# Optimization experiments

Measured on AMD Instinct MI355X. Metric: run time of the kernel, lower is better.

The kernel has to match this reference:

```python
import jax, jax.numpy as jnp
import numpy as np

B, I, H, MS, M = 8192, 1024, 1024, 64, 16
TAU = 1.0


def setup_inputs() -> dict:
    key = jax.random.key(0)
    ks = jax.random.split(key, 24)
    s = 0.02
    eps = 1e-6
    return {
        "x": jax.random.normal(ks[0], (B, I), jnp.float32),
        "h": jax.random.normal(ks[1], (B, H), jnp.float32),
        "c": jax.random.normal(ks[2], (B, H), jnp.float32),
        "memory": jax.random.normal(ks[3], (B, M, MS), jnp.float32),
        "u_gs": jax.random.uniform(ks[4], (B, M), jnp.float32, eps, 1.0 - eps),
        "u_a": jax.random.uniform(ks[5], (B, 1), jnp.float32, eps, 1.0 - eps),
        "u_b": jax.random.uniform(ks[6], (B, 1), jnp.float32, eps, 1.0 - eps),
        # pre-concatenated gate weights, matching torch.cat((W_x2*, W_h2*, W_c2*), 0)
        "W_i": jax.random.normal(ks[7], (I + 2 * H, H), jnp.float32) * s,
        "b_i": jnp.zeros((H,), jnp.float32),
        "W_f": jax.random.normal(ks[8], (I + 2 * H, H), jnp.float32) * s,
        "b_f": jnp.ones((H,), jnp.float32),
        "W_o": jax.random.normal(ks[9], (I + 2 * H, H), jnp.float32) * s,
        "b_o": jnp.zeros((H,), jnp.float32),
        "W_cand": jax.random.normal(ks[10], (I + H, H), jnp.float32) * s,
        "b_cand": jnp.zeros((H,), jnp.float32),
        "W_m": jax.random.normal(ks[11], (H, MS), jnp.float32) * s,
        "b_m": jnp.zeros((MS,), jnp.float32),
        "w_a_h": jax.random.normal(ks[12], (H, 1), jnp.float32) * s,
        "w_a_x": jax.random.normal(ks[13], (I, 1), jnp.float32) * s,
        "w_a_r": jax.random.normal(ks[14], (MS, 1), jnp.float32) * s,
        "w_b_h": jax.random.normal(ks[15], (H, 1), jnp.float32) * s,
        "w_b_x": jax.random.normal(ks[16], (I, 1), jnp.float32) * s,
        "w_b_r": jax.random.normal(ks[17], (MS, 1), jnp.float32) * s,
    }


def reference(x, h, c, memory, u_gs, u_a, u_b,
              W_i, b_i, W_f, b_f, W_o, b_o, W_cand, b_cand,
              W_m, b_m, w_a_h, w_a_x, w_a_r, w_b_h, w_b_x, w_b_r):
    # LSTM-style gates with peephole c in the concatenated input
    xhc = jnp.concatenate([x, h, c], axis=1)            # [B, I+2H]
    i = jax.nn.sigmoid(xhc @ W_i + b_i)
    f = jax.nn.sigmoid(xhc @ W_f + b_f)
    cp = jnp.tanh(jnp.concatenate([x, h], axis=1) @ W_cand + b_cand)
    c_new = f * c + i * cp
    o = jax.nn.sigmoid(jnp.concatenate([x, h, c_new], axis=1) @ W_o + b_o)
    h_new = o * jnp.tanh(c_new)

    # memory-slot attention with Gumbel-softmax sampling
    micro = h_new @ W_m + b_m                           # [B, MS]
    logits = jnp.einsum('bmk,bk->bm', memory, micro)    # [B, M]
    g = -jnp.log(-jnp.log(u_gs))                        # Gumbel(0,1)
    attn = jax.nn.softmax((logits + g) / TAU, axis=-1)  # sampled_locations
    sampled = jnp.einsum('bmk,bm->bk', memory, attn) + 1.0  # [B, MS]

    # gumbel-sigmoid (binary concrete) for alpha / beta
    la = jnp.log(u_a) - jnp.log1p(-u_a)
    lb = jnp.log(u_b) - jnp.log1p(-u_b)
    alpha = jax.nn.sigmoid((h_new @ w_a_h + x @ w_a_x + sampled @ w_a_r + la) / TAU)
    beta = jax.nn.sigmoid((h_new @ w_b_h + x @ w_b_x + sampled @ w_b_r + lb) / TAU)

    # [B, 2H+2]
    return jnp.concatenate([h_new, c_new, alpha, beta], axis=1)
```

## Files before the change

kernel.cpp:

```cpp
#include <hip/hip_runtime.h>

typedef __bf16 bfrag __attribute__((ext_vector_type(8)));
typedef float f32x4 __attribute__((ext_vector_type(4)));

#define GLDS16(g, l) __builtin_amdgcn_global_load_lds( \
    (__attribute__((address_space(1))) void*)(g),      \
    (__attribute__((address_space(3))) void*)(l), 16, 0, 0)

__device__ __forceinline__ float bf2f(ushort u) {
    return __uint_as_float(((unsigned)u) << 16);
}
__device__ __forceinline__ ushort f2bf(float f) {
    unsigned u = __float_as_uint(f);
    u += 0x7fff + ((u >> 16) & 1);
    return (ushort)(u >> 16);
}
__device__ __forceinline__ float sigmoidf_(float v) {
    return 1.0f / (1.0f + expf(-v));
}

struct TD { const float* src; ushort* dst; int src_ld; int dst_ld; int ktiles; int off; };
struct TA { TD d[6]; };

__global__ __launch_bounds__(256) void k_prep(const float* __restrict__ x,
                                              const float* __restrict__ h,
                                              const float* __restrict__ c,
                                              ushort* __restrict__ xhcb, TA a,
                                              const float* __restrict__ bi,
                                              const float* __restrict__ bf_,
                                              const float* __restrict__ bc,
                                              const float* __restrict__ bo,
                                              float* __restrict__ Biasf) {
    __shared__ float tile[64][65];
    int bid = blockIdx.x;
    int t = threadIdx.x;
    if (bid < 12288) {
        int idx = bid * 256 + t;
        int row = idx / 384;
        int c8 = (idx - row * 384) * 8;
        const float* s = (c8 < 1024) ? &x[(size_t)row * 1024 + c8]
                       : (c8 < 2048) ? &h[(size_t)row * 1024 + (c8 - 1024)]
                                     : &c[(size_t)row * 1024 + (c8 - 2048)];
        float4 va = *(const float4*)s;
        float4 vb = *(const float4*)(s + 4);
        ushort tmp[8] = {f2bf(va.x), f2bf(va.y), f2bf(va.z), f2bf(va.w),
                         f2bf(vb.x), f2bf(vb.y), f2bf(vb.z), f2bf(vb.w)};
        *(uint4*)&xhcb[(size_t)idx * 8] = *(uint4*)tmp;
    } else if (bid < 15120) {
        int tb = bid - 12288;
        int ri = 0;
#pragma unroll
        for (int i = 1; i < 6; ++i) ri = (tb >= a.d[i].off) ? i : ri;
        const float* src = a.d[ri].src;
        ushort* dst = a.d[ri].dst;
        int src_ld = a.d[ri].src_ld, dst_ld = a.d[ri].dst_ld;
        int local = tb - a.d[ri].off;
        int bx = local % a.d[ri].ktiles;
        int by = local / a.d[ri].ktiles;
        int k0 = bx * 64, n0 = by * 64;
        int c4 = (t & 15) * 4;
        int r = t >> 4;
#pragma unroll
        for (int i = 0; i < 4; ++i) {
            int rr = r + i * 16;
            float4 v = *(const float4*)&src[(size_t)(k0 + rr) * src_ld + n0 + c4];
            tile[rr][c4 + 0] = v.x; tile[rr][c4 + 1] = v.y;
            tile[rr][c4 + 2] = v.z; tile[rr][c4 + 3] = v.w;
        }
        __syncthreads();
        int kk8 = (t & 7) * 8;
        int nn = t >> 3;
#pragma unroll
        for (int i = 0; i < 2; ++i) {
            int n = nn + i * 32;
            ushort tmp[8];
#pragma unroll
            for (int j = 0; j < 8; ++j) tmp[j] = f2bf(tile[kk8 + j][n]);
            *(uint4*)&dst[(size_t)(n0 + n) * dst_ld + k0 + kk8] = *(uint4*)tmp;
        }
    } else {
        int idx = (bid - 15120) * 256 + t;
        int g = idx >> 10, n = idx & 1023;
        const float* s = (g == 0) ? bi : (g == 1) ? bf_ : (g == 2) ? bc : bo;
        Biasf[idx] = s[n];
    }
}

template <int KTOT>
__global__ __launch_bounds__(256) void k_gemm1t(const ushort* __restrict__ xhcb,
                                                const ushort* __restrict__ WT,
                                                const float* __restrict__ bias,
                                                ushort* __restrict__ Pre, int nbase) {
    __shared__ __align__(16) ushort As[128 * 64];
    __shared__ __align__(16) ushort Bs[128 * 64];
    int t = threadIdx.x;
    int m0 = blockIdx.x * 128, n0 = nbase + blockIdx.y * 128;
    int w = t >> 6, l = t & 63;
    int wm = (w & 1) * 64, wn = (w >> 1) * 64;
    int lane16 = l & 15, quad = l >> 4;
    int rowt = t >> 3;
    int kg = (t & 7) ^ (rowt & 7);
    int r7 = lane16 & 7;
    f32x4 acc[4][4] = {};

    const ushort* Abase = xhcb + (size_t)(m0 + rowt) * 3072 + kg * 8;
    const ushort* Bbase = WT + (size_t)(n0 + rowt) * 3072 + kg * 8;

    for (int k0 = 0; k0 < KTOT; k0 += 64) {
#pragma unroll
        for (int q = 0; q < 4; ++q)
            GLDS16(Abase + (size_t)q * 32 * 3072 + k0, As + q * 2048 + t * 8);
#pragma unroll
        for (int q = 0; q < 4; ++q)
            GLDS16(Bbase + (size_t)q * 32 * 3072 + k0, Bs + q * 2048 + t * 8);
        __syncthreads();
#pragma unroll
        for (int hh = 0; hh < 2; ++hh) {
            int slot8 = ((hh * 4 + quad) ^ r7) * 8;
            bfrag af[4], bfr[4];
#pragma unroll
            for (int i = 0; i < 4; ++i) {
                af[i]  = *(const bfrag*)&As[(wm + i * 16 + lane16) * 64 + slot8];
                bfr[i] = *(const bfrag*)&Bs[(wn + i * 16 + lane16) * 64 + slot8];
            }
#pragma unroll
            for (int i = 0; i < 4; ++i)
#pragma unroll
                for (int j = 0; j < 4; ++j)
                    acc[i][j] = __builtin_amdgcn_mfma_f32_16x16x32_bf16(af[i], bfr[j], acc[i][j], 0, 0, 0);
        }
        __syncthreads();
    }
#pragma unroll
    for (int i = 0; i < 4; ++i) {
#pragma unroll
        for (int j = 0; j < 4; ++j) {
            int col = n0 + wn + j * 16 + lane16;
            float bv = bias[col];
            int rbase = m0 + wm + i * 16 + quad * 4;
#pragma unroll
            for (int r = 0; r < 4; ++r)
                Pre[(size_t)(rbase + r) * 4096 + col] = f2bf(acc[i][j][r] + bv);
        }
    }
}

__global__ __launch_bounds__(256) void k_cnew(const ushort* __restrict__ Pre,
                                              const float* __restrict__ cin,
                                              ushort* __restrict__ Cnewb,
                                              float* __restrict__ out) {
    int idx8 = blockIdx.x * 256 + threadIdx.x;
    int b = idx8 >> 7;
    int n8 = (idx8 & 127) * 8;
    uint4 vi = *(const uint4*)(Pre + (size_t)b * 4096 + n8);
    uint4 vf = *(const uint4*)(Pre + (size_t)b * 4096 + 1024 + n8);
    uint4 vc = *(const uint4*)(Pre + (size_t)b * 4096 + 2048 + n8);
    float4 c0 = *(const float4*)(cin + (size_t)b * 1024 + n8);
    float4 c1 = *(const float4*)(cin + (size_t)b * 1024 + n8 + 4);
    const ushort* pi = (const ushort*)&vi;
    const ushort* pf = (const ushort*)&vf;
    const ushort* pc = (const ushort*)&vc;
    float cv[8] = {c0.x, c0.y, c0.z, c0.w, c1.x, c1.y, c1.z, c1.w};
    float cn[8];
    ushort cb[8];
#pragma unroll
    for (int j = 0; j < 8; ++j) {
        float iv = sigmoidf_(bf2f(pi[j]));
        float fv = sigmoidf_(bf2f(pf[j]));
        float cp = tanhf(bf2f(pc[j]));
        cn[j] = fv * cv[j] + iv * cp;
        cb[j] = f2bf(cn[j]);
    }
    *(uint4*)(Cnewb + (size_t)b * 1024 + n8) = *(uint4*)cb;
    float* orow = out + (size_t)b * 2050 + 1024 + n8;
#pragma unroll
    for (int j = 0; j < 4; ++j)
        *(float2*)(orow + j * 2) = make_float2(cn[j * 2], cn[j * 2 + 1]);
}

__global__ __launch_bounds__(256) void k_gemm2(const ushort* __restrict__ Cnewb,
                                               const ushort* __restrict__ WoCT,
                                               const ushort* __restrict__ Pre,
                                               ushort* __restrict__ Hnewb,
                                               float* __restrict__ out) {
    __shared__ __align__(16) ushort As[128 * 64];
    __shared__ __align__(16) ushort Bs[128 * 64];
    int t = threadIdx.x;
    int m0 = blockIdx.x * 128, n0 = blockIdx.y * 128;
    int w = t >> 6, l = t & 63;
    int wm = (w & 1) * 64, wn = (w >> 1) * 64;
    int lane16 = l & 15, quad = l >> 4;
    int rowt = t >> 3;
    int kg = (t & 7) ^ (rowt & 7);
    int r7 = lane16 & 7;
    f32x4 acc[4][4] = {};

    const ushort* Abase = Cnewb + (size_t)(m0 + rowt) * 1024 + kg * 8;
    const ushort* Bbase = WoCT + (size_t)(n0 + rowt) * 1024 + kg * 8;

    for (int k0 = 0; k0 < 1024; k0 += 64) {
#pragma unroll
        for (int q = 0; q < 4; ++q)
            GLDS16(Abase + (size_t)q * 32 * 1024 + k0, As + q * 2048 + t * 8);
#pragma unroll
        for (int q = 0; q < 4; ++q)
            GLDS16(Bbase + (size_t)q * 32 * 1024 + k0, Bs + q * 2048 + t * 8);
        __syncthreads();
#pragma unroll
        for (int hh = 0; hh < 2; ++hh) {
            int slot8 = ((hh * 4 + quad) ^ r7) * 8;
            bfrag af[4], bfr[4];
#pragma unroll
            for (int i = 0; i < 4; ++i) {
                af[i]  = *(const bfrag*)&As[(wm + i * 16 + lane16) * 64 + slot8];
                bfr[i] = *(const bfrag*)&Bs[(wn + i * 16 + lane16) * 64 + slot8];
            }
#pragma unroll
            for (int i = 0; i < 4; ++i)
#pragma unroll
                for (int j = 0; j < 4; ++j)
                    acc[i][j] = __builtin_amdgcn_mfma_f32_16x16x32_bf16(af[i], bfr[j], acc[i][j], 0, 0, 0);
        }
        __syncthreads();
    }
#pragma unroll
    for (int i = 0; i < 4; ++i) {
#pragma unroll
        for (int j = 0; j < 4; ++j) {
            int col = n0 + wn + j * 16 + lane16;
            int rbase = m0 + wm + i * 16 + quad * 4;
#pragma unroll
            for (int r = 0; r < 4; ++r) {
                int row = rbase + r;
                float opre = acc[i][j][r] + bf2f(Pre[(size_t)row * 4096 + 3072 + col]);
                float o = sigmoidf_(opre);
                float cnv = bf2f(Cnewb[(size_t)row * 1024 + col]);
                float hv = o * tanhf(cnv);
                Hnewb[(size_t)row * 1024 + col] = f2bf(hv);
                out[(size_t)row * 2050 + col] = hv;
            }
        }
    }
}

__global__ __launch_bounds__(256) void k_attn(
    const ushort* __restrict__ Hnewb, const float* __restrict__ outr,
    const float* __restrict__ x, const float* __restrict__ memory,
    const float* __restrict__ u_gs, const float* __restrict__ u_a,
    const float* __restrict__ u_b, const ushort* __restrict__ WmT,
    const float* __restrict__ b_m,
    const float* __restrict__ w_a_h, const float* __restrict__ w_a_x,
    const float* __restrict__ w_a_r, const float* __restrict__ w_b_h,
    const float* __restrict__ w_b_x, const float* __restrict__ w_b_r,
    float* __restrict__ out) {
    __shared__ float sMicro[16 * 64];
    __shared__ float sAttn[16 * 16];
    __shared__ float sSamp[16 * 64];

    int b0 = blockIdx.x * 16;
    int t = threadIdx.x;
    int w = t >> 6, l = t & 63;
    int lane16 = l & 15, quad = l >> 4;

    {
        f32x4 acc = {0.f, 0.f, 0.f, 0.f};
        const ushort* Ab = Hnewb + (size_t)(b0 + lane16) * 1024 + quad * 8;
        const ushort* Bb = WmT + (size_t)(w * 16 + lane16) * 1024 + quad * 8;
#pragma unroll 4
        for (int k0 = 0; k0 < 1024; k0 += 32) {
            bfrag av = *(const bfrag*)(Ab + k0);
            bfrag bv = *(const bfrag*)(Bb + k0);
            acc = __builtin_amdgcn_mfma_f32_16x16x32_bf16(av, bv, acc, 0, 0, 0);
        }
        float bm = b_m[w * 16 + lane16];
#pragma unroll
        for (int r = 0; r < 4; ++r)
            sMicro[(quad * 4 + r) * 64 + w * 16 + lane16] = acc[r] + bm;
    }
    __syncthreads();

    {
        int r = t >> 4, m = t & 15;
        const float4* mem4 = (const float4*)(memory + (size_t)(b0 + r) * 1024 + m * 64);
        float lg = 0.f;
#pragma unroll
        for (int k4 = 0; k4 < 16; ++k4) {
            float4 mv = mem4[k4];
            const float* sm = &sMicro[r * 64 + k4 * 4];
            lg += mv.x * sm[0] + mv.y * sm[1] + mv.z * sm[2] + mv.w * sm[3];
        }
        float u = u_gs[(b0 + r) * 16 + m];
        float z = lg - logf(-logf(u));
        float zm = z;
        for (int off = 8; off; off >>= 1) zm = fmaxf(zm, __shfl_xor(zm, off, 16));
        float p = expf(z - zm);
        float ps = p;
        for (int off = 8; off; off >>= 1) ps += __shfl_xor(ps, off, 16);
        sAttn[r * 16 + m] = p / ps;
    }
    __syncthreads();

#pragma unroll
    for (int q = 0; q < 4; ++q) {
        int r = w * 4 + q;
        const float* mem = memory + (size_t)(b0 + r) * 1024 + l;
        float s = 0.f;
#pragma unroll
        for (int m = 0; m < 16; ++m) s += sAttn[r * 16 + m] * mem[m * 64];
        sSamp[r * 64 + l] = s + 1.0f;
    }
    __syncthreads();

    {
        int r = t >> 4, s16 = t & 15;
        size_t hoff = (size_t)(b0 + r) * 2050;
        size_t xoff = (size_t)(b0 + r) * 1024;
        float za = 0.f, zb = 0.f;
        for (int kk = 0; kk < 64; ++kk) {
            int k = s16 + kk * 16;
            float hv = outr[hoff + k];
            float xv = x[xoff + k];
            za += hv * w_a_h[k] + xv * w_a_x[k];
            zb += hv * w_b_h[k] + xv * w_b_x[k];
        }
#pragma unroll
        for (int k = s16 * 4; k < s16 * 4 + 4; ++k) {
            float sv = sSamp[r * 64 + k];
            za += sv * w_a_r[k];
            zb += sv * w_b_r[k];
        }
        for (int off = 8; off; off >>= 1) {
            za += __shfl_xor(za, off, 16);
            zb += __shfl_xor(zb, off, 16);
        }
        if (s16 == 0) {
            float ua = u_a[b0 + r];
            float ub = u_b[b0 + r];
            float la = logf(ua) - log1pf(-ua);
            float lb = logf(ub) - log1pf(-ub);
            out[(size_t)(b0 + r) * 2050 + 2048] = sigmoidf_(za + la);
            out[(size_t)(b0 + r) * 2050 + 2049] = sigmoidf_(zb + lb);
        }
    }
}

extern "C" void kernel_launch(void* const* d_in, const int* in_sizes, int n_in,
                              void* d_out, int out_size, void* d_ws, size_t ws_size,
                              hipStream_t stream) {
    const float* x      = (const float*)d_in[0];
    const float* h      = (const float*)d_in[1];
    const float* c      = (const float*)d_in[2];
    const float* memory = (const float*)d_in[3];
    const float* u_gs   = (const float*)d_in[4];
    const float* u_a    = (const float*)d_in[5];
    const float* u_b    = (const float*)d_in[6];
    const float* W_i    = (const float*)d_in[7];
    const float* b_i    = (const float*)d_in[8];
    const float* W_f    = (const float*)d_in[9];
    const float* b_f    = (const float*)d_in[10];
    const float* W_o    = (const float*)d_in[11];
    const float* b_o    = (const float*)d_in[12];
    const float* W_cand = (const float*)d_in[13];
    const float* b_cand = (const float*)d_in[14];
    const float* W_m    = (const float*)d_in[15];
    const float* b_m    = (const float*)d_in[16];
    const float* w_a_h  = (const float*)d_in[17];
    const float* w_a_x  = (const float*)d_in[18];
    const float* w_a_r  = (const float*)d_in[19];
    const float* w_b_h  = (const float*)d_in[20];
    const float* w_b_x  = (const float*)d_in[21];
    const float* w_b_r  = (const float*)d_in[22];
    float* out = (float*)d_out;

    char* ws = (char*)d_ws;
    ushort* WT    = (ushort*)(ws);
    ushort* WoCT  = (ushort*)(ws + 25165824);
    ushort* Pre   = (ushort*)(ws + 27262976);
    ushort* xhcb  = (ushort*)(ws + 94371840);
    float*  Biasf = (float*)(ws + 144703488);
    ushort* WmT   = (ushort*)(ws + 144719872);
    ushort* Cnewb = xhcb;
    ushort* Hnewb = WT;

    TA ta;
    ta.d[0] = {W_i,                       WT,                        1024, 3072, 48, 0};
    ta.d[1] = {W_f,                       WT + (size_t)1024 * 3072,  1024, 3072, 48, 768};
    ta.d[2] = {W_cand,                    WT + (size_t)2048 * 3072,  1024, 3072, 32, 1536};
    ta.d[3] = {W_o,                       WT + (size_t)3072 * 3072,  1024, 3072, 32, 2048};
    ta.d[4] = {W_o + (size_t)2048 * 1024, WoCT,                      1024, 1024, 16, 2560};
    ta.d[5] = {W_m,                       WmT,                         64, 1024, 16, 2816};

    k_prep<<<15136, 256, 0, stream>>>(x, h, c, xhcb, ta, b_i, b_f, b_cand, b_o, Biasf);

    k_gemm1t<3072><<<dim3(64, 16), 256, 0, stream>>>(xhcb, WT, Biasf, Pre, 0);
    k_gemm1t<2048><<<dim3(64, 16), 256, 0, stream>>>(xhcb, WT, Biasf, Pre, 2048);
    k_cnew<<<4096, 256, 0, stream>>>(Pre, c, Cnewb, out);
    k_gemm2<<<dim3(64, 8), 256, 0, stream>>>(Cnewb, WoCT, Pre, Hnewb, out);
    k_attn<<<512, 256, 0, stream>>>(Hnewb, out, x, memory, u_gs, u_a, u_b, WmT, b_m,
                                    w_a_h, w_a_x, w_a_r, w_b_h, w_b_x, w_b_r, out);
}
```

Baseline: 522.2 us.

## Merge gate GEMMs into one 256x256-tile kernel with double-buffered LDS pipeline

Replaces the two 128x128-tile gate GEMM launches with a single 512-thread kernel using 256x256 tiles. The per-column K depth is chosen per block so both parts of the gate GEMM run in one grid. Global-to-LDS loads are double-buffered and issued in four phases interleaved with MFMA work, using explicit waitcnt, raw barriers and setprio to overlap memory with compute. Larger tiles raise data reuse, but they use 128KB of LDS per block and more accumulator registers, which limits occupancy, and the hand-placed waits are fragile.

After: 503.5 us. 3.6% less time.

```diff
diff --git a/kernel.cpp b/kernel.cpp
--- a/kernel.cpp
+++ b/kernel.cpp
@@ -86,61 +86,113 @@
     }
 }
 
-template <int KTOT>
-__global__ __launch_bounds__(256) void k_gemm1t(const ushort* __restrict__ xhcb,
-                                                const ushort* __restrict__ WT,
-                                                const float* __restrict__ bias,
-                                                ushort* __restrict__ Pre, int nbase) {
-    __shared__ __align__(16) ushort As[128 * 64];
-    __shared__ __align__(16) ushort Bs[128 * 64];
-    int t = threadIdx.x;
-    int m0 = blockIdx.x * 128, n0 = nbase + blockIdx.y * 128;
-    int w = t >> 6, l = t & 63;
-    int wm = (w & 1) * 64, wn = (w >> 1) * 64;
-    int lane16 = l & 15, quad = l >> 4;
-    int rowt = t >> 3;
-    int kg = (t & 7) ^ (rowt & 7);
-    int r7 = lane16 & 7;
-    f32x4 acc[4][4] = {};
-
-    const ushort* Abase = xhcb + (size_t)(m0 + rowt) * 3072 + kg * 8;
-    const ushort* Bbase = WT + (size_t)(n0 + rowt) * 3072 + kg * 8;
-
-    for (int k0 = 0; k0 < KTOT; k0 += 64) {
-#pragma unroll
-        for (int q = 0; q < 4; ++q)
-            GLDS16(Abase + (size_t)q * 32 * 3072 + k0, As + q * 2048 + t * 8);
-#pragma unroll
-        for (int q = 0; q < 4; ++q)
-            GLDS16(Bbase + (size_t)q * 32 * 3072 + k0, Bs + q * 2048 + t * 8);
-        __syncthreads();
-#pragma unroll
-        for (int hh = 0; hh < 2; ++hh) {
-            int slot8 = ((hh * 4 + quad) ^ r7) * 8;
-            bfrag af[4], bfr[4];
-#pragma unroll
-            for (int i = 0; i < 4; ++i) {
-                af[i]  = *(const bfrag*)&As[(wm + i * 16 + lane16) * 64 + slot8];
-                bfr[i] = *(const bfrag*)&Bs[(wn + i * 16 + lane16) * 64 + slot8];
-            }
-#pragma unroll
-            for (int i = 0; i < 4; ++i)
-#pragma unroll
-                for (int j = 0; j < 4; ++j)
-                    acc[i][j] = __builtin_amdgcn_mfma_f32_16x16x32_bf16(af[i], bfr[j], acc[i][j], 0, 0, 0);
-        }
-        __syncthreads();
-    }
-#pragma unroll
-    for (int i = 0; i < 4; ++i) {
-#pragma unroll
-        for (int j = 0; j < 4; ++j) {
-            int col = n0 + wn + j * 16 + lane16;
+__global__ __launch_bounds__(512) void k_gemm1(const ushort* __restrict__ xhcb,
+                                               const ushort* __restrict__ WT,
+                                               const float* __restrict__ bias,
+                                               ushort* __restrict__ Pre) {
+    __shared__ __align__(16) ushort lds[2][32768];
+    const int t = threadIdx.x;
+    const int m0 = blockIdx.x * 256;
+    const int by = blockIdx.y;
+    const int n0 = by * 256;
+    const int KTOT = (by < 8) ? 3072 : 2048;
+    const int NT = KTOT >> 6;
+    const int w = t >> 6, l = t & 63;
+    const int wr = w >> 2, wc = w & 3;
+    const int lane16 = l & 15, quad = l >> 4;
+    const int r7 = lane16 & 7;
+    const int rowt = t >> 3;
+    const int kg = (t & 7) ^ (rowt & 7);
+    const int brow_hi = rowt >> 5, brow_lo = rowt & 31;
+    f32x4 acc[8][4] = {};
+
+    const ushort* Ag = xhcb + (size_t)(m0 + rowt) * 3072 + kg * 8;
+    const ushort* Bg = WT + (size_t)(n0 + brow_lo) * 3072 + kg * 8;
+
+#define STAGE_A(BUF, PI, KT)                                                       \
+    do {                                                                           \
+        GLDS16(Ag + (size_t)((PI) * 64) * 3072 + (KT) * 64,                        \
+               &lds[BUF][((PI) * 64) * 64] + t * 8);                               \
+        GLDS16(Ag + (size_t)((PI) * 64 + 128) * 3072 + (KT) * 64,                  \
+               &lds[BUF][((PI) * 64 + 128) * 64] + t * 8);                         \
+    } while (0)
+
+#define STAGE_B(BUF, PI, KT)                                                       \
+    do {                                                                           \
+        GLDS16(Bg + (size_t)((PI) * 32 + brow_hi * 64) * 3072 + (KT) * 64,         \
+               &lds[BUF][16384 + ((PI) * 128) * 64] + t * 8);                      \
+        GLDS16(Bg + (size_t)((PI) * 32 + (2 + brow_hi) * 64) * 3072 + (KT) * 64,   \
+               &lds[BUF][16384 + ((PI) * 128 + 64) * 64] + t * 8);                 \
+    } while (0)
+
+#define PHASE(QM, QN, STAGE_CODE, TAIL_CODE)                                              \
+    do {                                                                                  \
+        bfrag af[4][2], bfv[2][2];                                                        \
+        _Pragma("unroll") for (int ii = 0; ii < 4; ++ii) {                                \
+            _Pragma("unroll") for (int h = 0; h < 2; ++h)                                 \
+                af[ii][h] = *(const bfrag*)&Acur[(wr * 128 + (QM) * 64 + ii * 16 + lane16) * 64 + \
+                                                 (((h * 4 + quad) ^ r7) * 8)];            \
+        }                                                                                 \
+        _Pragma("unroll") for (int jj = 0; jj < 2; ++jj) {                                \
+            _Pragma("unroll") for (int h = 0; h < 2; ++h)                                 \
+                bfv[jj][h] = *(const bfrag*)&Bcur[((QN) * 128 + wc * 32 + jj * 16 + lane16) * 64 + \
+                                                  (((h * 4 + quad) ^ r7) * 8)];           \
+        }                                                                                 \
+        STAGE_CODE;                                                                       \
+        __builtin_amdgcn_s_barrier();                                                     \
+        asm volatile("s_waitcnt lgkmcnt(0)" ::: "memory");                                \
+        __builtin_amdgcn_s_setprio(1);                                                    \
+        _Pragma("unroll") for (int ii = 0; ii < 4; ++ii) {                                \
+            _Pragma("unroll") for (int jj = 0; jj < 2; ++jj) {                            \
+                _Pragma("unroll") for (int h = 0; h < 2; ++h)                             \
+                    acc[(QM) * 4 + ii][(QN) * 2 + jj] =                                   \
+                        __builtin_amdgcn_mfma_f32_16x16x32_bf16(                          \
+                            af[ii][h], bfv[jj][h], acc[(QM) * 4 + ii][(QN) * 2 + jj],     \
+                            0, 0, 0);                                                     \
+            }                                                                             \
+        }                                                                                 \
+        __builtin_amdgcn_s_setprio(0);                                                    \
+        TAIL_CODE;                                                                        \
+        __builtin_amdgcn_s_barrier();                                                     \
+    } while (0)
+
+    STAGE_A(0, 0, 0); STAGE_B(0, 0, 0);
+    STAGE_A(0, 1, 0); STAGE_B(0, 1, 0);
+    STAGE_A(1, 0, 1); STAGE_B(1, 0, 1);
+    asm volatile("s_waitcnt vmcnt(4)" ::: "memory");
+    __builtin_amdgcn_s_barrier();
+
+    for (int kt = 0; kt < NT; ++kt) {
+        const int cur = kt & 1;
+        const int nxt = cur ^ 1;
+        const ushort* Acur = &lds[cur][0];
+        const ushort* Bcur = Acur + 16384;
+        PHASE(0, 0, { if (kt + 1 < NT) STAGE_A(nxt, 1, kt + 1); }, {});
+        PHASE(0, 1, { if (kt + 1 < NT) STAGE_B(nxt, 1, kt + 1); }, {});
+        PHASE(1, 0, { if (kt + 2 < NT) STAGE_A(cur, 0, kt + 2); }, {});
+        PHASE(1, 1, { if (kt + 2 < NT) STAGE_B(cur, 0, kt + 2); },
+              {
+                  if (kt + 2 < NT) {
+                      asm volatile("s_waitcnt vmcnt(4)" ::: "memory");
+                  } else if (kt + 1 < NT) {
+                      asm volatile("s_waitcnt vmcnt(0)" ::: "memory");
+                  }
+              });
+    }
+#undef PHASE
+#undef STAGE_A
+#undef STAGE_B
+
+#pragma unroll
+    for (int i = 0; i < 8; ++i) {
+#pragma unroll
+        for (int jj = 0; jj < 4; ++jj) {
+            int col = n0 + wc * 64 + (jj >> 1) * 32 + (jj & 1) * 16 + lane16;
             float bv = bias[col];
-            int rbase = m0 + wm + i * 16 + quad * 4;
+            int rbase = m0 + wr * 128 + i * 16 + quad * 4;
 #pragma unroll
             for (int r = 0; r < 4; ++r)
-                Pre[(size_t)(rbase + r) * 4096 + col] = f2bf(acc[i][j][r] + bv);
+                Pre[(size_t)(rbase + r) * 4096 + col] = f2bf(acc[i][jj][r] + bv);
         }
     }
 }
@@ -392,8 +444,7 @@
 
     k_prep<<<15136, 256, 0, stream>>>(x, h, c, xhcb, ta, b_i, b_f, b_cand, b_o, Biasf);
 
-    k_gemm1t<3072><<<dim3(64, 16), 256, 0, stream>>>(xhcb, WT, Biasf, Pre, 0);
-    k_gemm1t<2048><<<dim3(64, 16), 256, 0, stream>>>(xhcb, WT, Biasf, Pre, 2048);
+    k_gemm1<<<dim3(32, 16), 512, 0, stream>>>(xhcb, WT, Biasf, Pre);
     k_cnew<<<4096, 256, 0, stream>>>(Pre, c, Cnewb, out);
     k_gemm2<<<dim3(64, 8), 256, 0, stream>>>(Cnewb, WoCT, Pre, Hnewb, out);
     k_attn<<<512, 256, 0, stream>>>(Hnewb, out, x, memory, u_gs, u_a, u_b, WmT, b_m,
```
